# Performance work log

Hardware: AMD Instinct MI355X
Metric: run time of the kernel (lower is better)

Reference implementation:

```python
import jax, jax.numpy as jnp
import numpy as np

B, S, D, H = 2, 2048, 1024, 16
HD = D // H  # head_dim = 64


def setup_inputs() -> dict:
    key = jax.random.key(0)
    ks = jax.random.split(key, 12)
    scale = 1.0 / np.sqrt(D)
    inp = {
        "query": jax.random.normal(ks[0], (B, S, D), jnp.float32),
        "key": jax.random.normal(ks[1], (B, S, D), jnp.float32),
        "value": jax.random.normal(ks[2], (B, S, D), jnp.float32),
        # causal mask, True = masked out; shape [B, q_len, k_len]
        "mask": jnp.broadcast_to(
            jnp.triu(jnp.ones((S, S), jnp.bool_), k=1), (B, S, S)
        ),
        "Wq": jax.random.normal(ks[3], (D, D), jnp.float32) * scale,
        "bq": jnp.zeros((D,), jnp.float32),
        "Wk": jax.random.normal(ks[4], (D, D), jnp.float32) * scale,
        "bk": jnp.zeros((D,), jnp.float32),
        "Wv": jax.random.normal(ks[5], (D, D), jnp.float32) * scale,
        "bv": jnp.zeros((D,), jnp.float32),
        "Wo": jax.random.normal(ks[6], (D, D), jnp.float32) * scale,
        "bo": jnp.zeros((D,), jnp.float32),
    }
    return inp


def _split_heads(x):
    b, s, _ = x.shape
    return x.reshape(b, s, H, HD).transpose(0, 2, 1, 3)  # [B,H,S,HD]


def reference(query, key, value, mask, Wq, bq, Wk, bk, Wv, bv, Wo, bo):
    # Linear layers use torch convention: y = x @ W.T + b, W is [out, in]
    q = _split_heads(query @ Wq.T + bq)
    k = _split_heads(key @ Wk.T + bk)
    v = _split_heads(value @ Wv.T + bv)
    scores = jnp.einsum("bhqd,bhkd->bhqk", q, k) / jnp.sqrt(jnp.float32(HD))
    # normalized mask [B,1,q,k]; True means masked
    scores = jnp.where(mask[:, None, :, :], jnp.finfo(scores.dtype).min, scores)
    attn = jax.nn.softmax(scores, axis=-1)  # dropout is identity in eval
    ctx = jnp.einsum("bhqk,bhkd->bhqd", attn, v)
    merged = ctx.transpose(0, 2, 1, 3).reshape(query.shape[0], -1, D)
    out = merged @ Wo.T + bo
    return out
```

## Files before the change

kernel.cpp:

```cpp
#include <hip/hip_runtime.h>

#define B_ 2
#define S_ 2048
#define D_ 1024
#define H_ 16
#define HD_ 64
#define M_ (B_ * S_)

typedef __bf16 bf16x8 __attribute__((ext_vector_type(8)));
typedef float f32x4 __attribute__((ext_vector_type(4)));

__device__ inline unsigned short f2bf(float f) {
    unsigned int u = __builtin_bit_cast(unsigned int, f);
    u += 0x7fffu + ((u >> 16) & 1u);
    return (unsigned short)(u >> 16);
}

__device__ inline void async_ld16(const unsigned short* g, unsigned short* l) {
    __builtin_amdgcn_global_load_lds(
        (const __attribute__((address_space(1))) unsigned int*)g,
        (__attribute__((address_space(3))) unsigned int*)l, 16, 0, 0);
}

__global__ __launch_bounds__(256) void cvt_all(
    const float* __restrict__ i0, const float* __restrict__ i1, const float* __restrict__ i2,
    const float* __restrict__ i3, const float* __restrict__ i4, const float* __restrict__ i5,
    const float* __restrict__ i6,
    unsigned short* __restrict__ o0, unsigned short* __restrict__ o1, unsigned short* __restrict__ o2,
    unsigned short* __restrict__ o3, unsigned short* __restrict__ o4, unsigned short* __restrict__ o5,
    unsigned short* __restrict__ o6, int nbig, int nsmall) {
    int z = blockIdx.y;
    const float* in = (z == 0) ? i0 : (z == 1) ? i1 : (z == 2) ? i2 : (z == 3) ? i3
                     : (z == 4) ? i4 : (z == 5) ? i5 : i6;
    unsigned short* out = (z == 0) ? o0 : (z == 1) ? o1 : (z == 2) ? o2 : (z == 3) ? o3
                         : (z == 4) ? o4 : (z == 5) ? o5 : o6;
    int n = (z < 3) ? nbig : nsmall;
    int i = (blockIdx.x * 256 + threadIdx.x) * 4;
    if (i >= n) return;
    float4 v = *(const float4*)(in + i);
    ushort4 o;
    o.x = f2bf(v.x); o.y = f2bf(v.y); o.z = f2bf(v.z); o.w = f2bf(v.w);
    *(ushort4*)(out + i) = o;
}

__device__ inline void gemm_compute(const unsigned short* __restrict__ A,
                                    const unsigned short* __restrict__ W,
                                    int K, int m0, int n0,
                                    unsigned short* As0, unsigned short* As1,
                                    unsigned short* Bs0, unsigned short* Bs1,
                                    f32x4 acc[4][4]) {
    const int t = threadIdx.x;
    const int lane = t & 63, wave = t >> 6;
    const int ml = lane & 15, quad = lane >> 4;
    const int wr = (wave >> 1) * 64, wc = (wave & 1) * 64;
    const int lrow = lane >> 3;
    const int gchunk = (lane & 7) ^ lrow;

    const f32x4 zero = {0.f, 0.f, 0.f, 0.f};
    for (int i = 0; i < 4; i++)
        for (int j = 0; j < 4; j++) acc[i][j] = zero;

    const int niter = K >> 6;

    auto issue = [&](int kt, unsigned short* As, unsigned short* Bs) {
        int k0 = kt << 6;
        for (int i = 0; i < 4; i++) {
            int r = wave * 32 + i * 8;
            async_ld16(A + (size_t)(m0 + r + lrow) * K + k0 + gchunk * 8, As + r * 64);
            async_ld16(W + (size_t)(n0 + r + lrow) * K + k0 + gchunk * 8, Bs + r * 64);
        }
    };

    issue(0, As0, Bs0);
    __syncthreads();

    for (int kt = 0; kt < niter; kt++) {
        unsigned short* As = (kt & 1) ? As1 : As0;
        unsigned short* Bs = (kt & 1) ? Bs1 : Bs0;
        if (kt + 1 < niter) issue(kt + 1, (kt & 1) ? As0 : As1, (kt & 1) ? Bs0 : Bs1);

        for (int kk = 0; kk < 2; ++kk) {
            bf16x8 af[4], bfr[4];
            for (int i = 0; i < 4; i++)
                af[i] = *(const bf16x8*)(As + (wr + i * 16 + ml) * 64 + (((kk * 4 + quad) ^ (ml & 7)) << 3));
            for (int j = 0; j < 4; j++)
                bfr[j] = *(const bf16x8*)(Bs + (wc + j * 16 + ml) * 64 + (((kk * 4 + quad) ^ (ml & 7)) << 3));
            for (int i = 0; i < 4; i++)
                for (int j = 0; j < 4; j++)
                    acc[i][j] = __builtin_amdgcn_mfma_f32_16x16x32_bf16(af[i], bfr[j], acc[i][j], 0, 0, 0);
        }
        __syncthreads();
    }
}

__global__ __launch_bounds__(256) void gemm_qkv(
    const unsigned short* __restrict__ xq, const unsigned short* __restrict__ xk,
    const unsigned short* __restrict__ xv,
    const unsigned short* __restrict__ wq, const unsigned short* __restrict__ wk,
    const unsigned short* __restrict__ wv,
    const float* __restrict__ bq, const float* __restrict__ bk, const float* __restrict__ bv,
    unsigned short* __restrict__ oq, unsigned short* __restrict__ ok,
    unsigned short* __restrict__ ov) {
    extern __shared__ __align__(16) unsigned short smem[];
    unsigned short* As0 = smem;
    unsigned short* As1 = smem + 8192;
    unsigned short* Bs0 = smem + 16384;
    unsigned short* Bs1 = smem + 24576;

    const unsigned short *A, *W;
    const float* bias;
    unsigned short* out;
    int z = blockIdx.z;
    if (z == 0) { A = xq; W = wq; bias = bq; out = oq; }
    else if (z == 1) { A = xk; W = wk; bias = bk; out = ok; }
    else { A = xv; W = wv; bias = bv; out = ov; }

    int m0 = blockIdx.y * 128, n0 = blockIdx.x * 128;
    f32x4 acc[4][4];
    gemm_compute(A, W, D_, m0, n0, As0, As1, Bs0, Bs1, acc);

    const int t = threadIdx.x, lane = t & 63, wave = t >> 6;
    const int ml = lane & 15, quad = lane >> 4;
    const int wr = (wave >> 1) * 64, wc = (wave & 1) * 64;

    unsigned short* Cs = smem;
    const float sc = (z == 0) ? 0.125f : 1.0f;
    for (int i = 0; i < 4; i++)
        for (int j = 0; j < 4; j++) {
            int col = wc + j * 16 + ml;
            float bb = bias[n0 + col];
            for (int rg = 0; rg < 4; rg++) {
                int row = wr + i * 16 + quad * 4 + rg;
                unsigned short v = f2bf((acc[i][j][rg] + bb) * sc);
                if (z < 2) Cs[row * 136 + col] = v;
                else       Cs[col * 136 + row] = v;
            }
        }
    __syncthreads();

    const int r = t >> 1, hf = t & 1;
    if (z < 2) {
        unsigned short* dst = out + (size_t)(m0 + r) * D_ + n0 + hf * 64;
        const unsigned short* src = Cs + r * 136 + hf * 64;
        for (int i = 0; i < 8; i++)
            *(uint4*)(dst + i * 8) = *(const uint4*)(src + i * 8);
    } else {
        int n = n0 + r, h = n >> 6, d = n & 63;
        int b = m0 >> 11, s0 = m0 & 2047;
        unsigned short* dst = ov + ((size_t)((b * H_ + h) * 64 + d)) * S_ + s0 + hf * 64;
        const unsigned short* src = Cs + r * 136 + hf * 64;
        for (int i = 0; i < 8; i++)
            *(uint4*)(dst + i * 8) = *(const uint4*)(src + i * 8);
    }
}

__global__ __launch_bounds__(256) void gemm_out(const unsigned short* __restrict__ A,
                                                const unsigned short* __restrict__ W,
                                                const float* __restrict__ bias,
                                                float* __restrict__ out) {
    __shared__ unsigned short As0[128 * 64], As1[128 * 64], Bs0[128 * 64], Bs1[128 * 64];
    int m0 = blockIdx.y * 128, n0 = blockIdx.x * 128;
    f32x4 acc[4][4];
    gemm_compute(A, W, D_, m0, n0, As0, As1, Bs0, Bs1, acc);

    const int t = threadIdx.x, lane = t & 63, wave = t >> 6;
    const int ml = lane & 15, quad = lane >> 4;
    const int wr = (wave >> 1) * 64, wc = (wave & 1) * 64;
    for (int i = 0; i < 4; i++)
        for (int j = 0; j < 4; j++) {
            int n = n0 + wc + j * 16 + ml;
            float bb = bias[n];
            for (int rg = 0; rg < 4; rg++) {
                int m = m0 + wr + i * 16 + quad * 4 + rg;
                out[(size_t)m * D_ + n] = acc[i][j][rg] + bb;
            }
        }
}

__global__ __launch_bounds__(256, 2) void attn_kernel(const unsigned short* __restrict__ qm,
                                                      const unsigned short* __restrict__ km,
                                                      const unsigned short* __restrict__ vt,
                                                      unsigned short* __restrict__ ctx) {
    __shared__ unsigned short Ks[2][128 * 64];
    __shared__ unsigned short Vs[2][64 * 128];

    const int qb = 31 - (blockIdx.x >> 5);
    const int bh = blockIdx.x & 31;
    const int b = bh >> 4, h = bh & 15;
    const size_t vbase = (size_t)bh * S_ * 64;
    const int t = threadIdx.x, lane = t & 63, wave = t >> 6;
    const int ml = lane & 15, quad = lane >> 4;
    const int lrow = lane >> 3;
    const int gchunk = (lane & 7) ^ lrow;
    const int vrow = lane >> 4;
    const int q0 = qb * 64;

    bf16x8 qf[2];
    {
        int qrow = q0 + wave * 16 + ml;
        const unsigned short* qp = qm + (size_t)(b * S_ + qrow) * D_ + h * 64;
        qf[0] = *(const bf16x8*)(qp + quad * 8);
        qf[1] = *(const bf16x8*)(qp + 32 + quad * 8);
    }

    const f32x4 zero = {0.f, 0.f, 0.f, 0.f};
    f32x4 acc[4];
    for (int j = 0; j < 4; j++) acc[j] = zero;
    float m_i = -INFINITY, l_i = 0.f;

    const int ntiles = (qb + 2) >> 1;

    auto issue_tile = [&](int kt, int bb) {
        for (int i = 0; i < 4; i++) {
            int r = wave * 32 + i * 8;
            async_ld16(km + (size_t)(b * S_ + kt * 128 + r + lrow) * D_ + h * 64 + gchunk * 8,
                       Ks[bb] + r * 64);
            int dd = wave * 16 + i * 4;
            int d = dd + vrow;
            async_ld16(vt + vbase + (size_t)d * S_ + kt * 128 + (((lane & 15) ^ (d & 15)) << 3),
                       Vs[bb] + dd * 128);
        }
    };

    issue_tile(0, 0);
    __syncthreads();

    for (int kt = 0; kt < ntiles; kt++) {
        const int buf = kt & 1;
        if (kt + 1 < ntiles) issue_tile(kt + 1, buf ^ 1);

        f32x4 sacc[8];
        for (int n = 0; n < 8; n++) sacc[n] = zero;
        for (int n = 0; n < 8; n++)
            for (int kk = 0; kk < 2; kk++) {
                bf16x8 kf = *(const bf16x8*)(Ks[buf] + (n * 16 + ml) * 64 +
                                             (((kk * 4 + quad) ^ (ml & 7)) << 3));
                sacc[n] = __builtin_amdgcn_mfma_f32_16x16x32_bf16(kf, qf[kk], sacc[n], 0, 0, 0);
            }

        const bool last = (kt == ntiles - 1);
        const int qidx = q0 + wave * 16 + ml;
        if (last) {
            for (int n = 0; n < 8; n++)
                for (int rg = 0; rg < 4; rg++) {
                    int kidx = kt * 128 + n * 16 + quad * 4 + rg;
                    if (kidx > qidx) sacc[n][rg] = -3.0e38f;
                }
        }

        float mx = sacc[0][0];
        for (int n = 0; n < 8; n++)
            for (int rg = 0; rg < 4; rg++) mx = fmaxf(mx, sacc[n][rg]);
        mx = fmaxf(mx, __shfl_xor(mx, 16));
        mx = fmaxf(mx, __shfl_xor(mx, 32));
        float mc = fmaxf(m_i, mx);
        float al = __expf(m_i - mc);
        m_i = mc;
        float rs = 0.f;
        for (int n = 0; n < 8; n++)
            for (int rg = 0; rg < 4; rg++) {
                float p = __expf(sacc[n][rg] - mc);
                sacc[n][rg] = p;
                rs += p;
            }
        rs += __shfl_xor(rs, 16);
        rs += __shfl_xor(rs, 32);
        l_i = l_i * al + rs;

        float alT[4];
        for (int rg = 0; rg < 4; rg++) alT[rg] = __shfl(al, quad * 4 + rg);
        for (int j = 0; j < 4; j++)
            for (int rg = 0; rg < 4; rg++) acc[j][rg] *= alT[rg];

        for (int n2 = 0; n2 < 4; n2++) {
            union { bf16x8 v; unsigned short u[8]; } pk;
            for (int rg = 0; rg < 4; rg++) {
                pk.u[rg] = f2bf(sacc[2 * n2][rg]);
                pk.u[4 + rg] = f2bf(sacc[2 * n2 + 1][rg]);
            }
            const int c0 = 4 * n2 + (quad >> 1);
            const int qo = (quad & 1) << 2;
            for (int j = 0; j < 4; j++) {
                int row = j * 16 + ml;
                union { bf16x8 v; uint2 d2[2]; } vv;
                vv.d2[0] = *(const uint2*)(Vs[buf] + row * 128 + (((c0 ^ (row & 15)) << 3) + qo));
                vv.d2[1] = *(const uint2*)(Vs[buf] + row * 128 + ((((c0 + 2) ^ (row & 15)) << 3) + qo));
                acc[j] = __builtin_amdgcn_mfma_f32_16x16x32_bf16(pk.v, vv.v, acc[j], 0, 0, 0);
            }
        }

        __syncthreads();
    }

    float lT[4];
    for (int rg = 0; rg < 4; rg++) lT[rg] = __shfl(l_i, quad * 4 + rg);
    for (int j = 0; j < 4; j++) {
        int d = j * 16 + ml;
        for (int rg = 0; rg < 4; rg++) {
            int srow = q0 + wave * 16 + quad * 4 + rg;
            float val = acc[j][rg] / lT[rg];
            ctx[((size_t)(b * S_ + srow)) * D_ + h * 64 + d] = f2bf(val);
        }
    }
}

extern "C" void kernel_launch(void* const* d_in, const int* in_sizes, int n_in,
                              void* d_out, int out_size, void* d_ws, size_t ws_size,
                              hipStream_t stream) {
    const float* query = (const float*)d_in[0];
    const float* key_ = (const float*)d_in[1];
    const float* value = (const float*)d_in[2];
    const float* Wq = (const float*)d_in[4];
    const float* bq = (const float*)d_in[5];
    const float* Wk = (const float*)d_in[6];
    const float* bk = (const float*)d_in[7];
    const float* Wv = (const float*)d_in[8];
    const float* bv = (const float*)d_in[9];
    const float* Wo = (const float*)d_in[10];
    const float* bo = (const float*)d_in[11];
    float* out = (float*)d_out;

    const size_t XE = (size_t)M_ * D_;
    const size_t WE = (size_t)D_ * D_;
    char* ws = (char*)d_ws;
    unsigned short* xq = (unsigned short*)ws; ws += XE * 2;
    unsigned short* xk = (unsigned short*)ws; ws += XE * 2;
    unsigned short* xv = (unsigned short*)ws; ws += XE * 2;
    unsigned short* wqb = (unsigned short*)ws; ws += WE * 2;
    unsigned short* wkb = (unsigned short*)ws; ws += WE * 2;
    unsigned short* wvb = (unsigned short*)ws; ws += WE * 2;
    unsigned short* wob = (unsigned short*)ws; ws += WE * 2;
    unsigned short* qmb = (unsigned short*)ws; ws += XE * 2;
    unsigned short* kmb = (unsigned short*)ws; ws += XE * 2;
    unsigned short* vt = (unsigned short*)ws; ws += XE * 2;
    unsigned short* ctx = (unsigned short*)ws; ws += XE * 2;

    cvt_all<<<dim3(XE / 1024, 7), 256, 0, stream>>>(
        query, key_, value, Wq, Wk, Wv, Wo,
        xq, xk, xv, wqb, wkb, wvb, wob, (int)XE, (int)WE);

    gemm_qkv<<<dim3(D_ / 128, M_ / 128, 3), 256, 65536, stream>>>(
        xq, xk, xv, wqb, wkb, wvb, bq, bk, bv, qmb, kmb, vt);

    attn_kernel<<<dim3(1024), 256, 0, stream>>>(qmb, kmb, vt, ctx);

    gemm_out<<<dim3(D_ / 128, M_ / 128), 256, 0, stream>>>(ctx, wob, bo, out);
}
```

Baseline: 248.5 us.

## Load V directly from global, use exp2 softmax, packed bf16 cvt, raise occupancy

Drops the LDS staging of V in the attention kernel. Each lane now reads its V fragments straight from global memory (L2), which halves shared memory use, and launch bounds go from 2 to 4 blocks per CU. Softmax switches to exp2, with log2(e) folded into the Q scale, and P is packed with v_cvt_pk_bf16_f32. The kernel also raises wave priority around the QK MFMAs and replaces the final divide with rcp. The uncoalesced 8-byte global V loads sit on the critical path without any prefetch, which risks stalls that may outweigh the occupancy and ALU savings.

Result: slower. 356.1 us (+43.3%).

```diff
diff --git a/kernel.cpp b/kernel.cpp
--- a/kernel.cpp
+++ b/kernel.cpp
@@ -15,6 +15,14 @@
     u += 0x7fffu + ((u >> 16) & 1u);
     return (unsigned short)(u >> 16);
 }
+
+__device__ inline unsigned int cvt_pk_bf16(float lo, float hi) {
+    unsigned int r;
+    asm("v_cvt_pk_bf16_f32 %0, %1, %2" : "=v"(r) : "v"(lo), "v"(hi));
+    return r;
+}
+
+__device__ inline float fexp2(float x) { return __builtin_amdgcn_exp2f(x); }
 
 __device__ inline void async_ld16(const unsigned short* g, unsigned short* l) {
     __builtin_amdgcn_global_load_lds(
@@ -124,7 +132,7 @@
     const int wr = (wave >> 1) * 64, wc = (wave & 1) * 64;
 
     unsigned short* Cs = smem;
-    const float sc = (z == 0) ? 0.125f : 1.0f;
+    const float sc = (z == 0) ? 0.1803368801111204f : 1.0f;
     for (int i = 0; i < 4; i++)
         for (int j = 0; j < 4; j++) {
             int col = wc + j * 16 + ml;
@@ -177,12 +185,11 @@
         }
 }
 
-__global__ __launch_bounds__(256, 2) void attn_kernel(const unsigned short* __restrict__ qm,
+__global__ __launch_bounds__(256, 4) void attn_kernel(const unsigned short* __restrict__ qm,
                                                       const unsigned short* __restrict__ km,
                                                       const unsigned short* __restrict__ vt,
                                                       unsigned short* __restrict__ ctx) {
     __shared__ unsigned short Ks[2][128 * 64];
-    __shared__ unsigned short Vs[2][64 * 128];
 
     const int qb = 31 - (blockIdx.x >> 5);
     const int bh = blockIdx.x & 31;
@@ -192,7 +199,6 @@
     const int ml = lane & 15, quad = lane >> 4;
     const int lrow = lane >> 3;
     const int gchunk = (lane & 7) ^ lrow;
-    const int vrow = lane >> 4;
     const int q0 = qb * 64;
 
     bf16x8 qf[2];
@@ -203,6 +209,10 @@
         qf[1] = *(const bf16x8*)(qp + 32 + quad * 8);
     }
 
+    const unsigned short* vrow[4];
+    for (int j = 0; j < 4; j++)
+        vrow[j] = vt + vbase + (size_t)(j * 16 + ml) * S_ + ((quad & 1) << 2);
+
     const f32x4 zero = {0.f, 0.f, 0.f, 0.f};
     f32x4 acc[4];
     for (int j = 0; j < 4; j++) acc[j] = zero;
@@ -215,10 +225,6 @@
             int r = wave * 32 + i * 8;
             async_ld16(km + (size_t)(b * S_ + kt * 128 + r + lrow) * D_ + h * 64 + gchunk * 8,
                        Ks[bb] + r * 64);
-            int dd = wave * 16 + i * 4;
-            int d = dd + vrow;
-            async_ld16(vt + vbase + (size_t)d * S_ + kt * 128 + (((lane & 15) ^ (d & 15)) << 3),
-                       Vs[bb] + dd * 128);
         }
     };
 
@@ -231,12 +237,14 @@
 
         f32x4 sacc[8];
         for (int n = 0; n < 8; n++) sacc[n] = zero;
+        __builtin_amdgcn_s_setprio(1);
         for (int n = 0; n < 8; n++)
             for (int kk = 0; kk < 2; kk++) {
                 bf16x8 kf = *(const bf16x8*)(Ks[buf] + (n * 16 + ml) * 64 +
                                              (((kk * 4 + quad) ^ (ml & 7)) << 3));
                 sacc[n] = __builtin_amdgcn_mfma_f32_16x16x32_bf16(kf, qf[kk], sacc[n], 0, 0, 0);
             }
+        __builtin_amdgcn_s_setprio(0);
 
         const bool last = (kt == ntiles - 1);
         const int qidx = q0 + wave * 16 + ml;
@@ -254,12 +262,12 @@
         mx = fmaxf(mx, __shfl_xor(mx, 16));
         mx = fmaxf(mx, __shfl_xor(mx, 32));
         float mc = fmaxf(m_i, mx);
-        float al = __expf(m_i - mc);
+        float al = fexp2(m_i - mc);
         m_i = mc;
         float rs = 0.f;
         for (int n = 0; n < 8; n++)
             for (int rg = 0; rg < 4; rg++) {
-                float p = __expf(sacc[n][rg] - mc);
+                float p = fexp2(sacc[n][rg] - mc);
                 sacc[n][rg] = p;
                 rs += p;
             }
@@ -272,19 +280,18 @@
         for (int j = 0; j < 4; j++)
             for (int rg = 0; rg < 4; rg++) acc[j][rg] *= alT[rg];
 
+        const int kshift = kt * 128;
         for (int n2 = 0; n2 < 4; n2++) {
-            union { bf16x8 v; unsigned short u[8]; } pk;
-            for (int rg = 0; rg < 4; rg++) {
-                pk.u[rg] = f2bf(sacc[2 * n2][rg]);
-                pk.u[4 + rg] = f2bf(sacc[2 * n2 + 1][rg]);
-            }
+            union { bf16x8 v; unsigned int w[4]; } pk;
+            pk.w[0] = cvt_pk_bf16(sacc[2 * n2][0], sacc[2 * n2][1]);
+            pk.w[1] = cvt_pk_bf16(sacc[2 * n2][2], sacc[2 * n2][3]);
+            pk.w[2] = cvt_pk_bf16(sacc[2 * n2 + 1][0], sacc[2 * n2 + 1][1]);
+            pk.w[3] = cvt_pk_bf16(sacc[2 * n2 + 1][2], sacc[2 * n2 + 1][3]);
             const int c0 = 4 * n2 + (quad >> 1);
-            const int qo = (quad & 1) << 2;
             for (int j = 0; j < 4; j++) {
-                int row = j * 16 + ml;
                 union { bf16x8 v; uint2 d2[2]; } vv;
-                vv.d2[0] = *(const uint2*)(Vs[buf] + row * 128 + (((c0 ^ (row & 15)) << 3) + qo));
-                vv.d2[1] = *(const uint2*)(Vs[buf] + row * 128 + ((((c0 + 2) ^ (row & 15)) << 3) + qo));
+                vv.d2[0] = *(const uint2*)(vrow[j] + kshift + (c0 << 3));
+                vv.d2[1] = *(const uint2*)(vrow[j] + kshift + ((c0 + 2) << 3));
                 acc[j] = __builtin_amdgcn_mfma_f32_16x16x32_bf16(pk.v, vv.v, acc[j], 0, 0, 0);
             }
         }
@@ -292,14 +299,13 @@
         __syncthreads();
     }
 
-    float lT[4];
-    for (int rg = 0; rg < 4; rg++) lT[rg] = __shfl(l_i, quad * 4 + rg);
+    float inv[4];
+    for (int rg = 0; rg < 4; rg++) inv[rg] = __builtin_amdgcn_rcpf(__shfl(l_i, quad * 4 + rg));
     for (int j = 0; j < 4; j++) {
         int d = j * 16 + ml;
         for (int rg = 0; rg < 4; rg++) {
             int srow = q0 + wave * 16 + quad * 4 + rg;
-            float val = acc[j][rg] / lT[rg];
-            ctx[((size_t)(b * S_ + srow)) * D_ + h * 64 + d] = f2bf(val);
+            ctx[((size_t)(b * S_ + srow)) * D_ + h * 64 + d] = f2bf(acc[j][rg] * inv[rg]);
         }
     }
 }
```
